# Optimization experiments

Measured on AMD Instinct MI355X. Metric: run time of the kernel, lower is better.

Reference implementation:

```python
import jax, jax.numpy as jnp
import numpy as np

B, C, CI, H, W = 8, 256, 128, 64, 64
EPS = 1e-5

def conv1x1(x, w, b):
    # x: [B,C,H,W], w: [O,C], b: [O]
    return jnp.einsum('bchw,oc->bohw', x, w) + b[None, :, None, None]

def avgpool2(x):
    b, c, h, w = x.shape
    return x.reshape(b, c, h // 2, 2, w // 2, 2).mean(axis=(3, 5))

def setup_inputs() -> dict:
    key = jax.random.key(0)
    ks = jax.random.split(key, 16)
    s = lambda fan: 1.0 / np.sqrt(fan)
    inp = {
        'q': jax.random.normal(ks[0], (B, C, H, W), jnp.float32),
        'k': jax.random.normal(ks[1], (B, C, H, W), jnp.float32),
        'v': jax.random.normal(ks[2], (B, C, H, W), jnp.float32),
        'Wg':  jax.random.normal(ks[3], (CI, C), jnp.float32) * s(C),
        'bg':  jax.random.normal(ks[4], (CI,), jnp.float32) * s(C),
        'Wth': jax.random.normal(ks[5], (CI, C), jnp.float32) * s(C),
        'bth': jax.random.normal(ks[6], (CI,), jnp.float32) * s(C),
        'Wph': jax.random.normal(ks[7], (CI, C), jnp.float32) * s(C),
        'bph': jax.random.normal(ks[8], (CI,), jnp.float32) * s(C),
        'Ww':  jax.random.normal(ks[9], (C, CI), jnp.float32) * s(CI),
        'bw':  jax.random.normal(ks[10], (C,), jnp.float32) * s(CI),
        'gamma': jax.random.normal(ks[11], (C,), jnp.float32) * 0.1 + 1.0,
        'beta':  jax.random.normal(ks[12], (C,), jnp.float32) * 0.1,
        'mean':  jax.random.normal(ks[13], (C,), jnp.float32) * 0.1,
        'var':   jax.random.uniform(ks[14], (C,), jnp.float32, 0.5, 1.5),
    }
    return inp

def reference(q, k, v, Wg, bg, Wth, bth, Wph, bph, Ww, bw, gamma, beta, mean, var):
    b = q.shape[0]
    # g branch on v, phi branch on q: 1x1 conv then 2x2 avg-pool (sub_sample)
    g_x = avgpool2(conv1x1(v, Wg, bg)).reshape(b, CI, -1)            # [B,CI,M]
    g_x = g_x.transpose(0, 2, 1)                                      # [B,M,CI]
    theta_x = conv1x1(k, Wth, bth).reshape(b, CI, -1).transpose(0, 2, 1)  # [B,N,CI]
    phi_x = avgpool2(conv1x1(q, Wph, bph)).reshape(b, CI, -1)        # [B,CI,M]
    f = jnp.einsum('bnc,bcm->bnm', theta_x, phi_x)                   # [B,N,M]
    f_div_C = jax.nn.softmax(f, axis=-1)
    y = jnp.einsum('bnm,bmc->bnc', f_div_C, g_x)                     # [B,N,CI]
    y = y.transpose(0, 2, 1).reshape(b, CI, H, W)
    W_y = conv1x1(y, Ww, bw)
    # BatchNorm2d (inference form)
    W_y = (W_y - mean[None, :, None, None]) * (gamma[None, :, None, None]
            * jax.lax.rsqrt(var + EPS)[None, :, None, None]) + beta[None, :, None, None]
    return W_y + v
```

## Files before the change

kernel.cpp:

```cpp
#include <hip/hip_runtime.h>
#include <cstddef>

typedef unsigned short u16;
typedef unsigned int u32;
typedef __attribute__((ext_vector_type(8))) __bf16 bf16x8;
typedef __attribute__((ext_vector_type(4))) float f32x4;

constexpr int kB = 8, kC = 256, kCI = 128, kN = 4096, kM = 1024;
constexpr float kEPS = 1e-5f;

__device__ __forceinline__ u16 f2bf(float f) {
    u32 u = __float_as_uint(f);
    u32 r = (u + 0x7fffu + ((u >> 16) & 1u)) >> 16;
    return (u16)r;
}

__global__ __launch_bounds__(256) void prep_kernel(const float* __restrict__ Wth,
                                                   const float* __restrict__ Wph,
                                                   const float* __restrict__ Wg,
                                                   const float* __restrict__ Ww,
                                                   const float* __restrict__ bw,
                                                   const float* __restrict__ gamma,
                                                   const float* __restrict__ beta,
                                                   const float* __restrict__ mean,
                                                   const float* __restrict__ var,
                                                   u16* __restrict__ Wthb,
                                                   u16* __restrict__ Wphb,
                                                   u16* __restrict__ Wgb,
                                                   u16* __restrict__ Wwsb,
                                                   float* __restrict__ bb) {
    int idx = blockIdx.x * 256 + threadIdx.x;
    if (idx < 32768) {
        Wthb[idx] = f2bf(Wth[idx]);
    } else if (idx < 65536) {
        int j = idx - 32768; Wphb[j] = f2bf(Wph[j]);
    } else if (idx < 98304) {
        int j = idx - 65536; Wgb[j] = f2bf(Wg[j]);
    } else {
        int j = idx - 98304;
        int co = j >> 7;
        float sc = gamma[co] * rsqrtf(var[co] + kEPS);
        Wwsb[j] = f2bf(Ww[j] * sc);
        if ((j & 127) == 0) bb[co] = (bw[co] - mean[co]) * sc + beta[co];
    }
}

template <int CMAJOR, int POOL>
__global__ __launch_bounds__(256) void convp_kernel(const float* __restrict__ x,
                                                    const u16* __restrict__ Wb,
                                                    const float* __restrict__ bias,
                                                    u16* __restrict__ out, int Mn) {
    __shared__ __align__(16) u16 w_lds[128 * 72];
    __shared__ __align__(16) u16 x_lds[64 * 64];
    int t = threadIdx.x, b = blockIdx.y, n0 = blockIdx.x * 64;
    int w = t >> 6, lane = t & 63, l15 = lane & 15, quad = lane >> 4;
    int xn = t & 63, cbb = (t >> 6) * 2;

    f32x4 acc[8];
#pragma unroll
    for (int i = 0; i < 8; i++) acc[i] = (f32x4){0.f, 0.f, 0.f, 0.f};

    for (int c0 = 0; c0 < kC; c0 += 64) {
        __syncthreads();
#pragma unroll
        for (int i = 0; i < 4; i++) {
            int u = t + 256 * i;
            int ci = u >> 3, blk = u & 7;
            *(uint4*)&w_lds[ci * 72 + blk * 8] =
                *(const uint4*)&Wb[ci * kC + c0 + blk * 8];
        }
#pragma unroll
        for (int cc = 0; cc < 2; cc++) {
            int cb = cbb + cc;
            float f[8];
            if (POOL) {
                int p = n0 + xn, ph_ = p >> 5, pw_ = p & 31;
#pragma unroll
                for (int j = 0; j < 8; j++) {
                    const float* src = x + ((size_t)(b * kC + c0 + cb * 8 + j) * 64
                                            + 2 * ph_) * 64 + 2 * pw_;
                    float2 a = *(const float2*)src;
                    float2 b2 = *(const float2*)(src + 64);
                    f[j] = 0.25f * (a.x + a.y + b2.x + b2.y);
                }
            } else {
#pragma unroll
                for (int j = 0; j < 8; j++)
                    f[j] = x[(size_t)(b * kC + c0 + cb * 8 + j) * Mn + n0 + xn];
            }
            uint4 pk;
            pk.x = (u32)f2bf(f[0]) | ((u32)f2bf(f[1]) << 16);
            pk.y = (u32)f2bf(f[2]) | ((u32)f2bf(f[3]) << 16);
            pk.z = (u32)f2bf(f[4]) | ((u32)f2bf(f[5]) << 16);
            pk.w = (u32)f2bf(f[6]) | ((u32)f2bf(f[7]) << 16);
            *(uint4*)&x_lds[xn * 64 + ((cb ^ (xn & 7)) * 8)] = pk;
        }
        __syncthreads();

#pragma unroll
        for (int ks = 0; ks < 2; ks++) {
            int px = w * 16 + l15;
            bf16x8 xf = *(const bf16x8*)&x_lds[px * 64 + (((ks * 4 + quad) ^ (px & 7)) * 8)];
#pragma unroll
            for (int ct = 0; ct < 8; ct++) {
                bf16x8 wf = *(const bf16x8*)&w_lds[(ct * 16 + l15) * 72 + ks * 32 + quad * 8];
                if (CMAJOR)
                    acc[ct] = __builtin_amdgcn_mfma_f32_16x16x32_bf16(xf, wf, acc[ct], 0, 0, 0);
                else
                    acc[ct] = __builtin_amdgcn_mfma_f32_16x16x32_bf16(wf, xf, acc[ct], 0, 0, 0);
            }
        }
    }

    if (CMAJOR == 0) {
        int px = n0 + w * 16 + l15;
#pragma unroll
        for (int ct = 0; ct < 8; ct++) {
            int ci0 = ct * 16 + quad * 4;
            uint2 pk;
            pk.x = (u32)f2bf(acc[ct][0] + bias[ci0 + 0]) |
                   ((u32)f2bf(acc[ct][1] + bias[ci0 + 1]) << 16);
            pk.y = (u32)f2bf(acc[ct][2] + bias[ci0 + 2]) |
                   ((u32)f2bf(acc[ct][3] + bias[ci0 + 3]) << 16);
            *(uint2*)&out[(size_t)(b * Mn + px) * kCI + ci0] = pk;
        }
    } else {
        int px = n0 + w * 16 + quad * 4;
#pragma unroll
        for (int ct = 0; ct < 8; ct++) {
            int ci = ct * 16 + l15;
            float bs = bias[ci];
            uint2 pk;
            pk.x = (u32)f2bf(acc[ct][0] + bs) | ((u32)f2bf(acc[ct][1] + bs) << 16);
            pk.y = (u32)f2bf(acc[ct][2] + bs) | ((u32)f2bf(acc[ct][3] + bs) << 16);
            *(uint2*)&out[(size_t)(b * kCI + ci) * Mn + px] = pk;
        }
    }
}

__global__ __launch_bounds__(128) void attn_kernel(const u16* __restrict__ theta,
                                                   const u16* __restrict__ phi,
                                                   const u16* __restrict__ g,
                                                   u16* __restrict__ y) {
    __shared__ __align__(16) u16 ph_lds[8192];
    __shared__ __align__(16) u16 g_lds[8192];
    __shared__ __align__(16) u16 p_lds[4096];

    int t = threadIdx.x, b = blockIdx.y, n0 = blockIdx.x * 64;
    int w = t >> 6, lane = t & 63, l15 = lane & 15, quad = lane >> 4;

    bf16x8 thf[2][4];
    const u16* thB = theta + ((size_t)(b * kN) + n0 + w * 32) * kCI;
#pragma unroll
    for (int nt = 0; nt < 2; nt++)
#pragma unroll
        for (int ks = 0; ks < 4; ks++)
            thf[nt][ks] = *(const bf16x8*)&thB[(size_t)(nt * 16 + l15) * kCI + ks * 32 + quad * 8];

    f32x4 oacc[8][2];
#pragma unroll
    for (int ct = 0; ct < 8; ct++) {
        oacc[ct][0] = (f32x4){0.f, 0.f, 0.f, 0.f};
        oacc[ct][1] = (f32x4){0.f, 0.f, 0.f, 0.f};
    }
    float m_[2] = {-1e30f, -1e30f}, l_[2] = {0.f, 0.f};

    const u16* phB = phi + (size_t)b * kM * kCI;
    const u16* gB  = g   + (size_t)b * kCI * kM;
    u16* pw = p_lds + w * 2048;

    for (int c0 = 0; c0 < kM; c0 += 64) {
        __syncthreads();
#pragma unroll
        for (int it = 0; it < 8; it++) {
            int u = t + 128 * it;
            int row = u >> 4, cb = u & 15;
            *(uint4*)&ph_lds[(cb >> 2) * 2048 + row * 32 + (cb & 3) * 8] =
                *(const uint4*)&phB[(size_t)(c0 + row) * kCI + cb * 8];
        }
#pragma unroll
        for (int it = 0; it < 8; it++) {
            int u = t + 128 * it;
            int ci = u >> 3, mb = u & 7;
            *(uint4*)&g_lds[(mb >> 2) * 4096 + ci * 32 + (mb & 3) * 8] =
                *(const uint4*)&gB[(size_t)ci * kM + c0 + mb * 8];
        }
        __syncthreads();

        f32x4 sacc[4][2];
#pragma unroll
        for (int mt = 0; mt < 4; mt++) {
            sacc[mt][0] = (f32x4){0.f, 0.f, 0.f, 0.f};
            sacc[mt][1] = (f32x4){0.f, 0.f, 0.f, 0.f};
        }
#pragma unroll
        for (int ks = 0; ks < 4; ks++)
#pragma unroll
            for (int mt = 0; mt < 4; mt++) {
                bf16x8 a = *(const bf16x8*)&ph_lds[ks * 2048 + (mt * 16 + l15) * 32 + quad * 8];
                sacc[mt][0] = __builtin_amdgcn_mfma_f32_16x16x32_bf16(a, thf[0][ks], sacc[mt][0], 0, 0, 0);
                sacc[mt][1] = __builtin_amdgcn_mfma_f32_16x16x32_bf16(a, thf[1][ks], sacc[mt][1], 0, 0, 0);
            }

#pragma unroll
        for (int nt = 0; nt < 2; nt++) {
            float mc = -1e30f;
#pragma unroll
            for (int mt = 0; mt < 4; mt++)
#pragma unroll
                for (int r = 0; r < 4; r++) mc = fmaxf(mc, sacc[mt][nt][r]);
            mc = fmaxf(mc, __shfl_xor(mc, 16, 64));
            mc = fmaxf(mc, __shfl_xor(mc, 32, 64));
            float mp = m_[nt];
            float mn = fmaxf(mp, mc);
            int resc = __any(mn != mp);
            float alpha = __expf(mp - mn);
            m_[nt] = mn;
            float rs = 0.f;
#pragma unroll
            for (int mt = 0; mt < 4; mt++)
#pragma unroll
                for (int r = 0; r < 4; r++) {
                    float p = __expf(sacc[mt][nt][r] - mn);
                    sacc[mt][nt][r] = p;
                    rs += p;
                }
            rs += __shfl_xor(rs, 16, 64);
            rs += __shfl_xor(rs, 32, 64);
            l_[nt] = l_[nt] * alpha + rs;
            if (resc) {
#pragma unroll
                for (int ct = 0; ct < 8; ct++)
#pragma unroll
                    for (int r = 0; r < 4; r++) oacc[ct][nt][r] *= alpha;
            }
#pragma unroll
            for (int mt = 0; mt < 4; mt++)
#pragma unroll
                for (int h = 0; h < 2; h++) {
                    u32 ue = __float_as_uint(sacc[mt][nt][2 * h]) + 0x8000u;
                    u32 uo = __float_as_uint(sacc[mt][nt][2 * h + 1]) + 0x8000u;
                    u32 d = (ue >> 16) | (uo & 0xffff0000u);
                    int m = mt * 16 + quad * 4 + 2 * h;
                    int off = ((m >> 5) * 2 + nt) * 512 + (((m >> 3) & 3) * 16 + l15) * 8 + (m & 7);
                    *(u32*)&pw[off] = d;
                }
        }

#pragma unroll
        for (int ks2 = 0; ks2 < 2; ks2++) {
            bf16x8 b0 = *(const bf16x8*)&pw[(ks2 * 2 + 0) * 512 + (quad * 16 + l15) * 8];
            bf16x8 b1 = *(const bf16x8*)&pw[(ks2 * 2 + 1) * 512 + (quad * 16 + l15) * 8];
#pragma unroll
            for (int ct = 0; ct < 8; ct++) {
                bf16x8 a = *(const bf16x8*)&g_lds[ks2 * 4096 + (ct * 16 + l15) * 32 + quad * 8];
                oacc[ct][0] = __builtin_amdgcn_mfma_f32_16x16x32_bf16(a, b0, oacc[ct][0], 0, 0, 0);
                oacc[ct][1] = __builtin_amdgcn_mfma_f32_16x16x32_bf16(a, b1, oacc[ct][1], 0, 0, 0);
            }
        }
    }

#pragma unroll
    for (int nt = 0; nt < 2; nt++) {
        float inv = 1.0f / l_[nt];
        int n = n0 + w * 32 + nt * 16 + l15;
        u16* yr = y + ((size_t)(b * kN) + n) * kCI + quad * 4;
#pragma unroll
        for (int ct = 0; ct < 8; ct++) {
            uint2 pk;
            pk.x = (u32)f2bf(oacc[ct][nt][0] * inv) | ((u32)f2bf(oacc[ct][nt][1] * inv) << 16);
            pk.y = (u32)f2bf(oacc[ct][nt][2] * inv) | ((u32)f2bf(oacc[ct][nt][3] * inv) << 16);
            *(uint2*)&yr[ct * 16] = pk;
        }
    }
}

__global__ __launch_bounds__(256) void final_kernel(const u16* __restrict__ y,
                                                    const u16* __restrict__ Wws,
                                                    const float* __restrict__ bb,
                                                    const float* __restrict__ v,
                                                    float* __restrict__ out) {
    __shared__ __align__(16) u16 y_lds[64 * 136];
    int t = threadIdx.x, b = blockIdx.y, n0 = blockIdx.x * 64;
    int w = t >> 6, lane = t & 63, l15 = lane & 15, quad = lane >> 4;

#pragma unroll
    for (int i = 0; i < 4; i++) {
        int u = t + 256 * i;
        int row = u >> 4, blk = u & 15;
        *(uint4*)&y_lds[row * 136 + blk * 8] =
            *(const uint4*)&y[(size_t)(b * kN + n0 + row) * kCI + blk * 8];
    }
    __syncthreads();

    bf16x8 af[4];
#pragma unroll
    for (int ks = 0; ks < 4; ks++)
        af[ks] = *(const bf16x8*)&y_lds[(w * 16 + l15) * 136 + ks * 32 + quad * 8];

#pragma unroll
    for (int ct = 0; ct < 16; ct++) {
        f32x4 a = (f32x4){0.f, 0.f, 0.f, 0.f};
#pragma unroll
        for (int ks = 0; ks < 4; ks++) {
            bf16x8 bf = *(const bf16x8*)&Wws[(ct * 16 + l15) * kCI + ks * 32 + quad * 8];
            a = __builtin_amdgcn_mfma_f32_16x16x32_bf16(af[ks], bf, a, 0, 0, 0);
        }
        int co = ct * 16 + l15;
        float bbv = bb[co];
        size_t base = (size_t)(b * kC + co) * kN + n0 + w * 16 + quad * 4;
        float4 vv = *(const float4*)&v[base];
        float4 ov;
        ov.x = a[0] + bbv + vv.x;
        ov.y = a[1] + bbv + vv.y;
        ov.z = a[2] + bbv + vv.z;
        ov.w = a[3] + bbv + vv.w;
        *(float4*)&out[base] = ov;
    }
}

extern "C" void kernel_launch(void* const* d_in, const int* in_sizes, int n_in,
                              void* d_out, int out_size, void* d_ws, size_t ws_size,
                              hipStream_t stream) {
    (void)in_sizes; (void)n_in; (void)out_size; (void)ws_size;
    const float* q     = (const float*)d_in[0];
    const float* k     = (const float*)d_in[1];
    const float* v     = (const float*)d_in[2];
    const float* Wg    = (const float*)d_in[3];
    const float* bg    = (const float*)d_in[4];
    const float* Wth   = (const float*)d_in[5];
    const float* bth   = (const float*)d_in[6];
    const float* Wph   = (const float*)d_in[7];
    const float* bph   = (const float*)d_in[8];
    const float* Ww    = (const float*)d_in[9];
    const float* bw    = (const float*)d_in[10];
    const float* gamma = (const float*)d_in[11];
    const float* beta  = (const float*)d_in[12];
    const float* mean  = (const float*)d_in[13];
    const float* var   = (const float*)d_in[14];
    float* out = (float*)d_out;

    u16* wsu = (u16*)d_ws;
    u16*   theta = wsu;
    u16*   phi   = theta + 4194304;
    u16*   gbuf  = phi + 1048576;
    u16*   ybuf  = gbuf + 1048576;
    u16*   Wthb  = ybuf + 4194304;
    u16*   Wphb  = Wthb + 32768;
    u16*   Wgb   = Wphb + 32768;
    u16*   Wwsb  = Wgb + 32768;
    float* bbuf  = (float*)(Wwsb + 32768);

    prep_kernel<<<dim3(512), 256, 0, stream>>>(Wth, Wph, Wg, Ww, bw, gamma, beta,
                                               mean, var, Wthb, Wphb, Wgb, Wwsb, bbuf);
    convp_kernel<0, 0><<<dim3(64, 8), 256, 0, stream>>>(k, Wthb, bth, theta, kN);
    convp_kernel<0, 1><<<dim3(16, 8), 256, 0, stream>>>(q, Wphb, bph, phi, kM);
    convp_kernel<1, 1><<<dim3(16, 8), 256, 0, stream>>>(v, Wgb, bg, gbuf, kM);
    attn_kernel<<<dim3(64, 8), 128, 0, stream>>>(theta, phi, gbuf, ybuf);
    final_kernel<<<dim3(64, 8), 256, 0, stream>>>(ybuf, Wwsb, bbuf, v, out);
}
```

Baseline: 270.8 us.

## Merge phi/g conv launches and split attention rows across four waves with swizzled LDS

```diff
diff --git a/kernel.cpp b/kernel.cpp
--- a/kernel.cpp
+++ b/kernel.cpp
@@ -45,14 +45,15 @@
     }
 }
 
-template <int CMAJOR, int POOL>
-__global__ __launch_bounds__(256) void convp_kernel(const float* __restrict__ x,
-                                                    const u16* __restrict__ Wb,
-                                                    const float* __restrict__ bias,
-                                                    u16* __restrict__ out, int Mn) {
+template <int POOL>
+__device__ __forceinline__ void conv_body(const float* __restrict__ x,
+                                          const u16* __restrict__ Wb,
+                                          const float* __restrict__ bias,
+                                          u16* __restrict__ out, int Mn,
+                                          int cmajor, int b, int n0) {
     __shared__ __align__(16) u16 w_lds[128 * 72];
     __shared__ __align__(16) u16 x_lds[64 * 64];
-    int t = threadIdx.x, b = blockIdx.y, n0 = blockIdx.x * 64;
+    int t = threadIdx.x;
     int w = t >> 6, lane = t & 63, l15 = lane & 15, quad = lane >> 4;
     int xn = t & 63, cbb = (t >> 6) * 2;
 
@@ -104,7 +105,7 @@
 #pragma unroll
             for (int ct = 0; ct < 8; ct++) {
                 bf16x8 wf = *(const bf16x8*)&w_lds[(ct * 16 + l15) * 72 + ks * 32 + quad * 8];
-                if (CMAJOR)
+                if (cmajor)
                     acc[ct] = __builtin_amdgcn_mfma_f32_16x16x32_bf16(xf, wf, acc[ct], 0, 0, 0);
                 else
                     acc[ct] = __builtin_amdgcn_mfma_f32_16x16x32_bf16(wf, xf, acc[ct], 0, 0, 0);
@@ -112,7 +113,7 @@
         }
     }
 
-    if (CMAJOR == 0) {
+    if (cmajor == 0) {
         int px = n0 + w * 16 + l15;
 #pragma unroll
         for (int ct = 0; ct < 8; ct++) {
@@ -138,7 +139,27 @@
     }
 }
 
-__global__ __launch_bounds__(128) void attn_kernel(const u16* __restrict__ theta,
+__global__ __launch_bounds__(256) void convth_kernel(const float* __restrict__ x,
+                                                     const u16* __restrict__ Wb,
+                                                     const float* __restrict__ bias,
+                                                     u16* __restrict__ out) {
+    conv_body<0>(x, Wb, bias, out, kN, 0, blockIdx.y, blockIdx.x * 64);
+}
+
+__global__ __launch_bounds__(256) void convpg_kernel(const float* __restrict__ q,
+                                                     const float* __restrict__ v,
+                                                     const u16* __restrict__ Wph,
+                                                     const u16* __restrict__ Wg,
+                                                     const float* __restrict__ bph,
+                                                     const float* __restrict__ bg,
+                                                     u16* __restrict__ phi,
+                                                     u16* __restrict__ g) {
+    int z = blockIdx.z;
+    conv_body<1>(z ? v : q, z ? Wg : Wph, z ? bg : bph, z ? g : phi,
+                 kM, z, blockIdx.y, blockIdx.x * 64);
+}
+
+__global__ __launch_bounds__(256) void attn_kernel(const u16* __restrict__ theta,
                                                    const u16* __restrict__ phi,
                                                    const u16* __restrict__ g,
                                                    u16* __restrict__ y) {
@@ -148,130 +169,115 @@
 
     int t = threadIdx.x, b = blockIdx.y, n0 = blockIdx.x * 64;
     int w = t >> 6, lane = t & 63, l15 = lane & 15, quad = lane >> 4;
-
-    bf16x8 thf[2][4];
-    const u16* thB = theta + ((size_t)(b * kN) + n0 + w * 32) * kCI;
-#pragma unroll
-    for (int nt = 0; nt < 2; nt++)
-#pragma unroll
-        for (int ks = 0; ks < 4; ks++)
-            thf[nt][ks] = *(const bf16x8*)&thB[(size_t)(nt * 16 + l15) * kCI + ks * 32 + quad * 8];
-
-    f32x4 oacc[8][2];
-#pragma unroll
-    for (int ct = 0; ct < 8; ct++) {
-        oacc[ct][0] = (f32x4){0.f, 0.f, 0.f, 0.f};
-        oacc[ct][1] = (f32x4){0.f, 0.f, 0.f, 0.f};
-    }
-    float m_[2] = {-1e30f, -1e30f}, l_[2] = {0.f, 0.f};
+    int sw = (l15 >> 1) & 3;
+
+    bf16x8 thf[4];
+    const u16* thB = theta + ((size_t)(b * kN) + n0 + w * 16 + l15) * kCI;
+#pragma unroll
+    for (int ks = 0; ks < 4; ks++)
+        thf[ks] = *(const bf16x8*)&thB[ks * 32 + quad * 8];
+
+    f32x4 oacc[8];
+#pragma unroll
+    for (int ct = 0; ct < 8; ct++) oacc[ct] = (f32x4){0.f, 0.f, 0.f, 0.f};
+    float m_ = -1e30f, l_ = 0.f;
 
     const u16* phB = phi + (size_t)b * kM * kCI;
     const u16* gB  = g   + (size_t)b * kCI * kM;
-    u16* pw = p_lds + w * 2048;
+    u16* pw = p_lds + w * 1024;
 
     for (int c0 = 0; c0 < kM; c0 += 64) {
         __syncthreads();
 #pragma unroll
-        for (int it = 0; it < 8; it++) {
-            int u = t + 128 * it;
+        for (int it = 0; it < 4; it++) {
+            int u = t + 256 * it;
             int row = u >> 4, cb = u & 15;
-            *(uint4*)&ph_lds[(cb >> 2) * 2048 + row * 32 + (cb & 3) * 8] =
+            *(uint4*)&ph_lds[(cb >> 2) * 2048 + row * 32 + (((cb & 3) ^ ((row >> 1) & 3)) * 8)] =
                 *(const uint4*)&phB[(size_t)(c0 + row) * kCI + cb * 8];
         }
 #pragma unroll
-        for (int it = 0; it < 8; it++) {
-            int u = t + 128 * it;
+        for (int it = 0; it < 4; it++) {
+            int u = t + 256 * it;
             int ci = u >> 3, mb = u & 7;
-            *(uint4*)&g_lds[(mb >> 2) * 4096 + ci * 32 + (mb & 3) * 8] =
+            *(uint4*)&g_lds[(mb >> 2) * 4096 + ci * 32 + (((mb & 3) ^ ((ci >> 1) & 3)) * 8)] =
                 *(const uint4*)&gB[(size_t)ci * kM + c0 + mb * 8];
         }
         __syncthreads();
 
-        f32x4 sacc[4][2];
-#pragma unroll
-        for (int mt = 0; mt < 4; mt++) {
-            sacc[mt][0] = (f32x4){0.f, 0.f, 0.f, 0.f};
-            sacc[mt][1] = (f32x4){0.f, 0.f, 0.f, 0.f};
-        }
+        f32x4 sacc[4];
+#pragma unroll
+        for (int mt = 0; mt < 4; mt++) sacc[mt] = (f32x4){0.f, 0.f, 0.f, 0.f};
 #pragma unroll
         for (int ks = 0; ks < 4; ks++)
 #pragma unroll
             for (int mt = 0; mt < 4; mt++) {
-                bf16x8 a = *(const bf16x8*)&ph_lds[ks * 2048 + (mt * 16 + l15) * 32 + quad * 8];
-                sacc[mt][0] = __builtin_amdgcn_mfma_f32_16x16x32_bf16(a, thf[0][ks], sacc[mt][0], 0, 0, 0);
-                sacc[mt][1] = __builtin_amdgcn_mfma_f32_16x16x32_bf16(a, thf[1][ks], sacc[mt][1], 0, 0, 0);
-            }
-
-#pragma unroll
-        for (int nt = 0; nt < 2; nt++) {
-            float mc = -1e30f;
-#pragma unroll
-            for (int mt = 0; mt < 4; mt++)
-#pragma unroll
-                for (int r = 0; r < 4; r++) mc = fmaxf(mc, sacc[mt][nt][r]);
-            mc = fmaxf(mc, __shfl_xor(mc, 16, 64));
-            mc = fmaxf(mc, __shfl_xor(mc, 32, 64));
-            float mp = m_[nt];
-            float mn = fmaxf(mp, mc);
-            int resc = __any(mn != mp);
-            float alpha = __expf(mp - mn);
-            m_[nt] = mn;
-            float rs = 0.f;
-#pragma unroll
-            for (int mt = 0; mt < 4; mt++)
-#pragma unroll
-                for (int r = 0; r < 4; r++) {
-                    float p = __expf(sacc[mt][nt][r] - mn);
-                    sacc[mt][nt][r] = p;
-                    rs += p;
-                }
-            rs += __shfl_xor(rs, 16, 64);
-            rs += __shfl_xor(rs, 32, 64);
-            l_[nt] = l_[nt] * alpha + rs;
-            if (resc) {
-#pragma unroll
-                for (int ct = 0; ct < 8; ct++)
-#pragma unroll
-                    for (int r = 0; r < 4; r++) oacc[ct][nt][r] *= alpha;
-            }
-#pragma unroll
-            for (int mt = 0; mt < 4; mt++)
-#pragma unroll
-                for (int h = 0; h < 2; h++) {
-                    u32 ue = __float_as_uint(sacc[mt][nt][2 * h]) + 0x8000u;
-                    u32 uo = __float_as_uint(sacc[mt][nt][2 * h + 1]) + 0x8000u;
-                    u32 d = (ue >> 16) | (uo & 0xffff0000u);
-                    int m = mt * 16 + quad * 4 + 2 * h;
-                    int off = ((m >> 5) * 2 + nt) * 512 + (((m >> 3) & 3) * 16 + l15) * 8 + (m & 7);
-                    *(u32*)&pw[off] = d;
-                }
-        }
+                bf16x8 a = *(const bf16x8*)&ph_lds[ks * 2048 + (mt * 16 + l15) * 32 +
+                                                   ((quad ^ sw) * 8)];
+                sacc[mt] = __builtin_amdgcn_mfma_f32_16x16x32_bf16(a, thf[ks], sacc[mt], 0, 0, 0);
+            }
+
+        float mc = -1e30f;
+#pragma unroll
+        for (int mt = 0; mt < 4; mt++)
+#pragma unroll
+            for (int r = 0; r < 4; r++) mc = fmaxf(mc, sacc[mt][r]);
+        mc = fmaxf(mc, __shfl_xor(mc, 16, 64));
+        mc = fmaxf(mc, __shfl_xor(mc, 32, 64));
+        float mn = fmaxf(m_, mc);
+        int resc = __any(mn != m_);
+        float alpha = __expf(m_ - mn);
+        m_ = mn;
+        float rs = 0.f;
+#pragma unroll
+        for (int mt = 0; mt < 4; mt++)
+#pragma unroll
+            for (int r = 0; r < 4; r++) {
+                float p = __expf(sacc[mt][r] - mn);
+                sacc[mt][r] = p;
+                rs += p;
+            }
+        rs += __shfl_xor(rs, 16, 64);
+        rs += __shfl_xor(rs, 32, 64);
+        l_ = l_ * alpha + rs;
+        if (resc) {
+#pragma unroll
+            for (int ct = 0; ct < 8; ct++)
+#pragma unroll
+                for (int r = 0; r < 4; r++) oacc[ct][r] *= alpha;
+        }
+#pragma unroll
+        for (int mt = 0; mt < 4; mt++)
+#pragma unroll
+            for (int h = 0; h < 2; h++) {
+                u32 d = (u32)f2bf(sacc[mt][2 * h]) | ((u32)f2bf(sacc[mt][2 * h + 1]) << 16);
+                int m = mt * 16 + quad * 4 + 2 * h;
+                int frag = m >> 5;
+                int kblk = ((m >> 3) & 3);
+                int j = (quad & 1) * 4 + 2 * h;
+                *(u32*)&pw[frag * 512 + l15 * 32 + ((kblk ^ sw) * 8) + j] = d;
+            }
 
 #pragma unroll
         for (int ks2 = 0; ks2 < 2; ks2++) {
-            bf16x8 b0 = *(const bf16x8*)&pw[(ks2 * 2 + 0) * 512 + (quad * 16 + l15) * 8];
-            bf16x8 b1 = *(const bf16x8*)&pw[(ks2 * 2 + 1) * 512 + (quad * 16 + l15) * 8];
+            bf16x8 bfrag = *(const bf16x8*)&pw[ks2 * 512 + l15 * 32 + ((quad ^ sw) * 8)];
 #pragma unroll
             for (int ct = 0; ct < 8; ct++) {
-                bf16x8 a = *(const bf16x8*)&g_lds[ks2 * 4096 + (ct * 16 + l15) * 32 + quad * 8];
-                oacc[ct][0] = __builtin_amdgcn_mfma_f32_16x16x32_bf16(a, b0, oacc[ct][0], 0, 0, 0);
-                oacc[ct][1] = __builtin_amdgcn_mfma_f32_16x16x32_bf16(a, b1, oacc[ct][1], 0, 0, 0);
-            }
-        }
-    }
-
-#pragma unroll
-    for (int nt = 0; nt < 2; nt++) {
-        float inv = 1.0f / l_[nt];
-        int n = n0 + w * 32 + nt * 16 + l15;
-        u16* yr = y + ((size_t)(b * kN) + n) * kCI + quad * 4;
-#pragma unroll
-        for (int ct = 0; ct < 8; ct++) {
-            uint2 pk;
-            pk.x = (u32)f2bf(oacc[ct][nt][0] * inv) | ((u32)f2bf(oacc[ct][nt][1] * inv) << 16);
-            pk.y = (u32)f2bf(oacc[ct][nt][2] * inv) | ((u32)f2bf(oacc[ct][nt][3] * inv) << 16);
-            *(uint2*)&yr[ct * 16] = pk;
-        }
+                bf16x8 a = *(const bf16x8*)&g_lds[ks2 * 4096 + (ct * 16 + l15) * 32 +
+                                                  ((quad ^ sw) * 8)];
+                oacc[ct] = __builtin_amdgcn_mfma_f32_16x16x32_bf16(a, bfrag, oacc[ct], 0, 0, 0);
+            }
+        }
+    }
+
+    float inv = 1.0f / l_;
+    int n = n0 + w * 16 + l15;
+    u16* yr = y + ((size_t)(b * kN) + n) * kCI + quad * 4;
+#pragma unroll
+    for (int ct = 0; ct < 8; ct++) {
+        uint2 pk;
+        pk.x = (u32)f2bf(oacc[ct][0] * inv) | ((u32)f2bf(oacc[ct][1] * inv) << 16);
+        pk.y = (u32)f2bf(oacc[ct][2] * inv) | ((u32)f2bf(oacc[ct][3] * inv) << 16);
+        *(uint2*)&yr[ct * 16] = pk;
     }
 }
 
@@ -353,9 +359,8 @@
 
     prep_kernel<<<dim3(512), 256, 0, stream>>>(Wth, Wph, Wg, Ww, bw, gamma, beta,
                                                mean, var, Wthb, Wphb, Wgb, Wwsb, bbuf);
-    convp_kernel<0, 0><<<dim3(64, 8), 256, 0, stream>>>(k, Wthb, bth, theta, kN);
-    convp_kernel<0, 1><<<dim3(16, 8), 256, 0, stream>>>(q, Wphb, bph, phi, kM);
-    convp_kernel<1, 1><<<dim3(16, 8), 256, 0, stream>>>(v, Wgb, bg, gbuf, kM);
-    attn_kernel<<<dim3(64, 8), 128, 0, stream>>>(theta, phi, gbuf, ybuf);
+    convth_kernel<<<dim3(64, 8), 256, 0, stream>>>(k, Wthb, bth, theta);
+    convpg_kernel<<<dim3(16, 8, 2), 256, 0, stream>>>(q, v, Wphb, Wgb, bph, bg, phi, gbuf);
+    attn_kernel<<<dim3(64, 8), 256, 0, stream>>>(theta, phi, gbuf, ybuf);
     final_kernel<<<dim3(64, 8), 256, 0, stream>>>(ybuf, Wwsb, bbuf, v, out);
 }
```

Result: faster. 254.2 us (-6.1%).
